# Optimization experiments

Measured on AMD Instinct MI355X. Metric: run time of the kernel, lower is better.

Reference implementation:

```python
import jax, jax.numpy as jnp
import numpy as np

S, B, L, D, H, NOP = 4, 8, 512, 128, 128, 64  # segments, batch, seg_len, input_dim, hidden, n_operators
W = S * L  # 2048 total words
FT = 0.1   # forget-gate floor


def _norm_mat(m):
    # divide each row by its count of nonzero entries (torch normalize_matrix)
    cnt = (m != 0).sum(-1, keepdims=True).astype(m.dtype)
    return m / (cnt + 1e-30)


def _l2(x):
    return x / (jnp.linalg.norm(x, axis=-1, keepdims=True) + 1e-30)


def setup_inputs() -> dict:
    key = jax.random.key(0)
    ks = jax.random.split(key, 16)
    word_outputs = jax.random.normal(ks[0], (S, B, L, D), jnp.float32)
    node_hidden = jax.random.normal(ks[1], (B, D), jnp.float32)
    op_embedding = jax.random.normal(ks[2], (B, NOP, D), jnp.float32)
    word_operator = (jax.random.uniform(ks[3], (B, W, NOP)) < 0.05).astype(jnp.float32)
    word_word = (jax.random.uniform(ks[4], (B, W, W)) < 0.02).astype(jnp.float32)
    depend_relation = (jax.random.uniform(ks[5], (S, B, L, L)) < 0.05).astype(jnp.float32)
    word_exist_matrix = (jax.random.uniform(ks[6], (B, W, W)) < 0.9).astype(jnp.float32)
    word_exist_sequence = (jax.random.uniform(ks[7], (B, W)) < 0.9).astype(jnp.float32)
    goal_word = (jax.random.uniform(ks[8], (B, W)) < 0.2).astype(jnp.float32)

    def lin(k, fi, fo):
        k1, k2 = jax.random.split(k)
        s = 1.0 / np.sqrt(fi).astype(np.float32)
        return (jax.random.uniform(k1, (fi, fo), jnp.float32, -s, s),
                jax.random.uniform(k2, (fo,), jnp.float32, -s, s))

    o_w_W, o_w_b = lin(ks[9], D, H)
    wk_W, wk_b = lin(ks[10], D, H)
    ws_W, ws_b = lin(ks[11], D, H)
    up_W, up_b = lin(ks[12], 3 * H, D)
    wg_W, wg_b = lin(ks[13], D, D)
    fg_W, fg_b = lin(ks[14], 2 * D, D)
    return dict(word_outputs=word_outputs, node_hidden=node_hidden, op_embedding=op_embedding,
                word_operator=word_operator, word_word=word_word, depend_relation=depend_relation,
                word_exist_matrix=word_exist_matrix, word_exist_sequence=word_exist_sequence,
                goal_word=goal_word, o_w_W=o_w_W, o_w_b=o_w_b, wk_W=wk_W, wk_b=wk_b,
                ws_W=ws_W, ws_b=ws_b, up_W=up_W, up_b=up_b, wg_W=wg_W, wg_b=wg_b,
                fg_W=fg_W, fg_b=fg_b)


def reference(word_outputs, node_hidden, op_embedding, word_operator, word_word,
              depend_relation, word_exist_matrix, word_exist_sequence, goal_word,
              o_w_W, o_w_b, wk_W, wk_b, ws_W, ws_b, up_W, up_b, wg_W, wg_b, fg_W, fg_b):
    # cat(word_outputs, dim=1) -> [B, W, D]
    all_word = word_outputs.transpose(1, 0, 2, 3).reshape(B, W, D)
    # operator aggregation: [B,W,NOP] @ o_w(op_embedding) -> [B,W,H], L2-normalized
    word_o = _l2(jnp.einsum('bwo,boh->bwh', word_operator, op_embedding @ o_w_W + o_w_b))
    # knowledge aggregation over masked word-word adjacency
    adj_k = _norm_mat(word_word * word_exist_matrix)
    word_w_k = _l2(jnp.einsum('bvw,bwh->bvh', adj_k, all_word @ wk_W + wk_b))
    # per-segment dependency aggregation, then concat along word dim
    seg = jnp.einsum('sbij,sbjh->sbih', _norm_mat(depend_relation), word_outputs @ ws_W + ws_b)
    word_w_s = _l2(seg.transpose(1, 0, 2, 3).reshape(B, W, H))
    neighbor = jnp.concatenate([word_o, word_w_k, word_w_s], axis=-1)  # [B, W, 3H]
    word_updated = jax.nn.relu(neighbor @ up_W + up_b)  # [B, W, D]
    # goal pooling: bmm([B,1,W],[B,W,D]) -> [B,D]
    gw = _norm_mat(goal_word * word_exist_sequence)
    goal_w = jnp.einsum('bw,bwd->bd', gw, word_updated)
    goal_updated = jax.nn.relu(goal_w @ wg_W + wg_b)
    forget = jax.nn.sigmoid(jnp.concatenate([goal_w, node_hidden], axis=-1) @ fg_W + fg_b)
    return jnp.maximum(forget, FT) * node_hidden + (1.0 - forget) * goal_updated
```

## Files before the change

kernel.cpp:

```cpp
#include <hip/hip_runtime.h>
#include <math.h>

#define Sn 4
#define Bn 8
#define Ln 512
#define Dn 128
#define Hn 128
#define NOPn 64
#define Wn 2048


__device__ __forceinline__ float bf2f(unsigned short u) {
    return __uint_as_float(((unsigned int)u) << 16);
}
__device__ __forceinline__ unsigned short f2bf(float f) {
    unsigned int u = __float_as_uint(f);
    return (unsigned short)((u + 0x7FFFu + ((u >> 16) & 1u)) >> 16);
}

__global__ __launch_bounds__(256) void prep_k(const float* __restrict__ A,
                                              const float* __restrict__ W1,
                                              const float* __restrict__ W2,
                                              const float* __restrict__ b1,
                                              const float* __restrict__ b2,
                                              unsigned short* __restrict__ C1,
                                              unsigned short* __restrict__ C2,
                                              const float* __restrict__ ope,
                                              const float* __restrict__ owW,
                                              const float* __restrict__ owb,
                                              unsigned short* __restrict__ oph,
                                              const float* __restrict__ goal,
                                              const float* __restrict__ wes,
                                              int* __restrict__ widx,
                                              int* __restrict__ wcnt) {
    __shared__ __align__(16) float lA[32][68];
    __shared__ __align__(16) float lW1[32][132];
    __shared__ __align__(16) float lW2[32][132];
    __shared__ int cnt;
    const int bid = blockIdx.x, tid = threadIdx.x;

    if (bid < 256) {
        const int m0 = bid * 64;
        float acc1[4][8] = {}, acc2[4][8] = {};
        const int r0 = (tid & 15) * 4;
        const int h0 = (tid >> 4) * 8;
        for (int k0 = 0; k0 < 128; k0 += 32) {
            __syncthreads();
            {
                const int r = tid >> 2, kk = (tid & 3) * 8;
                const float* src = A + (size_t)(m0 + r) * 128 + (k0 + kk);
                float4 v0 = reinterpret_cast<const float4*>(src)[0];
                float4 v1 = reinterpret_cast<const float4*>(src)[1];
                lA[kk + 0][r] = v0.x; lA[kk + 1][r] = v0.y;
                lA[kk + 2][r] = v0.z; lA[kk + 3][r] = v0.w;
                lA[kk + 4][r] = v1.x; lA[kk + 5][r] = v1.y;
                lA[kk + 6][r] = v1.z; lA[kk + 7][r] = v1.w;
            }
            {
                const int kk = tid >> 3, hh = (tid & 7) * 16;
                const float* s1 = W1 + (size_t)(k0 + kk) * 128 + hh;
                const float* s2 = W2 + (size_t)(k0 + kk) * 128 + hh;
#pragma unroll
                for (int q = 0; q < 4; ++q) {
                    float4 v1 = reinterpret_cast<const float4*>(s1)[q];
                    float4 v2 = reinterpret_cast<const float4*>(s2)[q];
                    lW1[kk][hh + 4 * q + 0] = v1.x; lW1[kk][hh + 4 * q + 1] = v1.y;
                    lW1[kk][hh + 4 * q + 2] = v1.z; lW1[kk][hh + 4 * q + 3] = v1.w;
                    lW2[kk][hh + 4 * q + 0] = v2.x; lW2[kk][hh + 4 * q + 1] = v2.y;
                    lW2[kk][hh + 4 * q + 2] = v2.z; lW2[kk][hh + 4 * q + 3] = v2.w;
                }
            }
            __syncthreads();
#pragma unroll
            for (int k = 0; k < 32; ++k) {
                float4 a   = *reinterpret_cast<const float4*>(&lA[k][r0]);
                float4 w10 = *reinterpret_cast<const float4*>(&lW1[k][h0]);
                float4 w11 = *reinterpret_cast<const float4*>(&lW1[k][h0 + 4]);
                float4 w20 = *reinterpret_cast<const float4*>(&lW2[k][h0]);
                float4 w21 = *reinterpret_cast<const float4*>(&lW2[k][h0 + 4]);
                float av[4] = {a.x, a.y, a.z, a.w};
                float wv1[8] = {w10.x, w10.y, w10.z, w10.w, w11.x, w11.y, w11.z, w11.w};
                float wv2[8] = {w20.x, w20.y, w20.z, w20.w, w21.x, w21.y, w21.z, w21.w};
#pragma unroll
                for (int i = 0; i < 4; ++i)
#pragma unroll
                    for (int j = 0; j < 8; ++j) {
                        acc1[i][j] = fmaf(av[i], wv1[j], acc1[i][j]);
                        acc2[i][j] = fmaf(av[i], wv2[j], acc2[i][j]);
                    }
            }
        }
#pragma unroll
        for (int i = 0; i < 4; ++i) {
            alignas(16) unsigned short u1[8], u2[8];
#pragma unroll
            for (int j = 0; j < 8; ++j) {
                u1[j] = f2bf(acc1[i][j] + b1[h0 + j]);
                u2[j] = f2bf(acc2[i][j] + b2[h0 + j]);
            }
            const size_t off = (size_t)(m0 + r0 + i) * 128 + h0;
            *reinterpret_cast<uint4*>(C1 + off) = *reinterpret_cast<const uint4*>(u1);
            *reinterpret_cast<uint4*>(C2 + off) = *reinterpret_cast<const uint4*>(u2);
        }
    } else if (bid < 264) {
        const int m0 = (bid - 256) * 64;
        float acc[4][8] = {};
        const int r0 = (tid & 15) * 4;
        const int h0 = (tid >> 4) * 8;
        for (int k0 = 0; k0 < 128; k0 += 32) {
            __syncthreads();
            {
                const int r = tid >> 2, kk = (tid & 3) * 8;
                const float* src = ope + (size_t)(m0 + r) * 128 + (k0 + kk);
                float4 v0 = reinterpret_cast<const float4*>(src)[0];
                float4 v1 = reinterpret_cast<const float4*>(src)[1];
                lA[kk + 0][r] = v0.x; lA[kk + 1][r] = v0.y;
                lA[kk + 2][r] = v0.z; lA[kk + 3][r] = v0.w;
                lA[kk + 4][r] = v1.x; lA[kk + 5][r] = v1.y;
                lA[kk + 6][r] = v1.z; lA[kk + 7][r] = v1.w;
            }
            {
                const int kk = tid >> 3, hh = (tid & 7) * 16;
                const float* src = owW + (size_t)(k0 + kk) * 128 + hh;
#pragma unroll
                for (int q = 0; q < 4; ++q) {
                    float4 v = reinterpret_cast<const float4*>(src)[q];
                    lW1[kk][hh + 4 * q + 0] = v.x; lW1[kk][hh + 4 * q + 1] = v.y;
                    lW1[kk][hh + 4 * q + 2] = v.z; lW1[kk][hh + 4 * q + 3] = v.w;
                }
            }
            __syncthreads();
#pragma unroll
            for (int k = 0; k < 32; ++k) {
                float4 a  = *reinterpret_cast<const float4*>(&lA[k][r0]);
                float4 w0 = *reinterpret_cast<const float4*>(&lW1[k][h0]);
                float4 w1 = *reinterpret_cast<const float4*>(&lW1[k][h0 + 4]);
                float av[4] = {a.x, a.y, a.z, a.w};
                float wv[8] = {w0.x, w0.y, w0.z, w0.w, w1.x, w1.y, w1.z, w1.w};
#pragma unroll
                for (int i = 0; i < 4; ++i)
#pragma unroll
                    for (int j = 0; j < 8; ++j) acc[i][j] = fmaf(av[i], wv[j], acc[i][j]);
            }
        }
#pragma unroll
        for (int i = 0; i < 4; ++i) {
            alignas(16) unsigned short us[8];
#pragma unroll
            for (int j = 0; j < 8; ++j) us[j] = f2bf(acc[i][j] + owb[h0 + j]);
            *reinterpret_cast<uint4*>(oph + (size_t)(m0 + r0 + i) * 128 + h0) =
                *reinterpret_cast<const uint4*>(us);
        }
    } else {
        const int b = bid - 264;
        if (tid == 0) cnt = 0;
        __syncthreads();
#pragma unroll
        for (int j = 0; j < 8; ++j) {
            const int w = tid * 8 + j;
            if (goal[b * Wn + w] != 0.f && wes[b * Wn + w] != 0.f) {
                const int p = atomicAdd(&cnt, 1);
                if (p < 1024) widx[b * 1024 + p] = w;
            }
        }
        __syncthreads();
        if (tid == 0) wcnt[b] = cnt < 1024 ? cnt : 1024;
    }
}

__global__ __launch_bounds__(256) void mega_agg(const int* __restrict__ widx,
                                                const int* __restrict__ wcnt,
                                                const float* __restrict__ ww,
                                                const float* __restrict__ wem,
                                                const float* __restrict__ dep,
                                                const float* __restrict__ wop,
                                                const unsigned short* __restrict__ oph,
                                                const unsigned short* __restrict__ wkh,
                                                const unsigned short* __restrict__ wsh,
                                                unsigned short* __restrict__ nbc) {
    const int slot = blockIdx.x;
    const int b = slot >> 10, i = slot & 1023;
    if (i >= wcnt[b]) return;
    const int w_dst = widx[slot];
    const int t = threadIdx.x;
    const int lane = t & 63, wv = t >> 6;

    __shared__ int kidx[512];
    __shared__ int keep[512];
    __shared__ int sidx[256];
    __shared__ int kn, sn;
    __shared__ float part1[4][128];
    __shared__ float part2[4][128];
    if (t == 0) { kn = 0; sn = 0; }
    __syncthreads();

    const float* wwr = ww + ((size_t)(b * Wn + w_dst)) * Wn;
#pragma unroll
    for (int q = 0; q < 2; ++q) {
        const int e0 = q * 1024 + t * 4;
        float4 v = *reinterpret_cast<const float4*>(wwr + e0);
        float vv[4] = {v.x, v.y, v.z, v.w};
#pragma unroll
        for (int j = 0; j < 4; ++j)
            if (vv[j] != 0.f) {
                int p = atomicAdd(&kn, 1);
                if (p < 512) kidx[p] = e0 + j;
            }
    }
    const int sD = w_dst >> 9, lD = w_dst & 511;
    if (t < 128) {
        const float* dr = dep + ((size_t)((sD * Bn + b) * Ln + lD)) * Ln + t * 4;
        float4 v = *reinterpret_cast<const float4*>(dr);
        float vv[4] = {v.x, v.y, v.z, v.w};
#pragma unroll
        for (int j = 0; j < 4; ++j)
            if (vv[j] != 0.f) {
                int p = atomicAdd(&sn, 1);
                if (p < 256) sidx[p] = t * 4 + j;
            }
    }
    float m_op = 0.f;
    if (wv == 3) m_op = wop[((size_t)(b * Wn + w_dst)) * NOPn + lane];
    __syncthreads();

    const int nk = kn < 512 ? kn : 512;
    const int ns = sn < 256 ? sn : 256;
    for (int p = t; p < nk; p += 256)
        keep[p] = (wem[((size_t)(b * Wn + w_dst)) * Wn + kidx[p]] != 0.f) ? 1 : 0;
    __syncthreads();

    {
        float a0 = 0.f, a1 = 0.f;
        for (int p = wv; p < nk; p += 4)
            if (keep[p]) {
                const int w = kidx[p];
                const int s = w >> 9, l = w & 511;
                ushort2 x = *reinterpret_cast<const ushort2*>(
                    wkh + ((size_t)((s * Bn + b) * Ln + l)) * Hn + 2 * lane);
                a0 += bf2f(x.x);
                a1 += bf2f(x.y);
            }
        part1[wv][2 * lane]     = a0;
        part1[wv][2 * lane + 1] = a1;
    }
    {
        const unsigned short* base = wsh + (size_t)((sD * Bn + b) * Ln) * Hn + 2 * lane;
        float a0 = 0.f, a1 = 0.f;
        for (int p = wv; p < ns; p += 4) {
            ushort2 x = *reinterpret_cast<const ushort2*>(base + (size_t)sidx[p] * Hn);
            a0 += bf2f(x.x);
            a1 += bf2f(x.y);
        }
        part2[wv][2 * lane]     = a0;
        part2[wv][2 * lane + 1] = a1;
    }
    if (wv == 3) {
        unsigned long long bal = __ballot(m_op != 0.f);
        float a0 = 0.f, a1 = 0.f;
        const unsigned short* base = oph + (size_t)b * NOPn * Hn + 2 * lane;
        while (bal) {
            const int o = __ffsll(bal) - 1;
            bal &= bal - 1;
            ushort2 v = *reinterpret_cast<const ushort2*>(base + o * Hn);
            a0 += bf2f(v.x);
            a1 += bf2f(v.y);
        }
        float ss = a0 * a0 + a1 * a1;
#pragma unroll
        for (int off = 1; off < 64; off <<= 1) ss += __shfl_xor(ss, off);
        const float sc = 1.f / (sqrtf(ss) + 1e-30f);
        ushort2 o2 = {f2bf(a0 * sc), f2bf(a1 * sc)};
        *reinterpret_cast<ushort2*>(nbc + (size_t)slot * 384 + 2 * lane) = o2;
    }
    __syncthreads();

    if (wv == 0) {
        float s0 = 0.f, s1 = 0.f;
#pragma unroll
        for (int q = 0; q < 4; ++q) {
            s0 += part1[q][2 * lane];
            s1 += part1[q][2 * lane + 1];
        }
        float ss = s0 * s0 + s1 * s1;
#pragma unroll
        for (int off = 1; off < 64; off <<= 1) ss += __shfl_xor(ss, off);
        const float sc = 1.f / (sqrtf(ss) + 1e-30f);
        ushort2 o2 = {f2bf(s0 * sc), f2bf(s1 * sc)};
        *reinterpret_cast<ushort2*>(nbc + (size_t)slot * 384 + 128 + 2 * lane) = o2;
    } else if (wv == 1) {
        float s0 = 0.f, s1 = 0.f;
#pragma unroll
        for (int q = 0; q < 4; ++q) {
            s0 += part2[q][2 * lane];
            s1 += part2[q][2 * lane + 1];
        }
        float ss = s0 * s0 + s1 * s1;
#pragma unroll
        for (int off = 1; off < 64; off <<= 1) ss += __shfl_xor(ss, off);
        const float sc = 1.f / (sqrtf(ss) + 1e-30f);
        ushort2 o2 = {f2bf(s0 * sc), f2bf(s1 * sc)};
        *reinterpret_cast<ushort2*>(nbc + (size_t)slot * 384 + 256 + 2 * lane) = o2;
    }
}

__global__ __launch_bounds__(256) void up_gemm_c(const unsigned short* __restrict__ A,
                                                 const float* __restrict__ Wm,
                                                 const float* __restrict__ bias,
                                                 const int* __restrict__ wcnt,
                                                 float* __restrict__ C) {
    const int m0 = blockIdx.x * 64;
    if ((m0 & 1023) >= wcnt[m0 >> 10]) return;
    __shared__ __align__(16) float lA[32][68];
    __shared__ __align__(16) float lW[32][132];
    const int tid = threadIdx.x;
    float acc[4][8] = {};
    const int r0 = (tid & 15) * 4;
    const int h0 = (tid >> 4) * 8;
    for (int k0 = 0; k0 < 384; k0 += 32) {
        __syncthreads();
        {
            const int r = tid >> 2, kk = (tid & 3) * 8;
            const unsigned short* src = A + (size_t)(m0 + r) * 384 + (k0 + kk);
            alignas(16) unsigned short us[8];
            *reinterpret_cast<uint4*>(us) = *reinterpret_cast<const uint4*>(src);
#pragma unroll
            for (int j = 0; j < 8; ++j) lA[kk + j][r] = bf2f(us[j]);
        }
        {
            const int kk = tid >> 3, hh = (tid & 7) * 16;
            const float* src = Wm + (size_t)(k0 + kk) * 128 + hh;
#pragma unroll
            for (int q = 0; q < 4; ++q) {
                float4 v = reinterpret_cast<const float4*>(src)[q];
                lW[kk][hh + 4 * q + 0] = v.x; lW[kk][hh + 4 * q + 1] = v.y;
                lW[kk][hh + 4 * q + 2] = v.z; lW[kk][hh + 4 * q + 3] = v.w;
            }
        }
        __syncthreads();
#pragma unroll
        for (int k = 0; k < 32; ++k) {
            float4 a  = *reinterpret_cast<const float4*>(&lA[k][r0]);
            float4 w0 = *reinterpret_cast<const float4*>(&lW[k][h0]);
            float4 w1 = *reinterpret_cast<const float4*>(&lW[k][h0 + 4]);
            float av[4] = {a.x, a.y, a.z, a.w};
            float wv[8] = {w0.x, w0.y, w0.z, w0.w, w1.x, w1.y, w1.z, w1.w};
#pragma unroll
            for (int i = 0; i < 4; ++i)
#pragma unroll
                for (int j = 0; j < 8; ++j) acc[i][j] = fmaf(av[i], wv[j], acc[i][j]);
        }
    }
#pragma unroll
    for (int i = 0; i < 4; ++i) {
        float o[8];
#pragma unroll
        for (int j = 0; j < 8; ++j) o[j] = fmaxf(acc[i][j] + bias[h0 + j], 0.f);
        float* dst = C + (size_t)(m0 + r0 + i) * 128 + h0;
        *reinterpret_cast<float4*>(dst)     = reinterpret_cast<float4&>(o[0]);
        *reinterpret_cast<float4*>(dst + 4) = reinterpret_cast<float4&>(o[4]);
    }
}

__global__ __launch_bounds__(1024) void final3_k(const int* __restrict__ wcnt,
                                                 const float* __restrict__ wuc,
                                                 const float* __restrict__ nh,
                                                 const float* __restrict__ wgW,
                                                 const float* __restrict__ wgb,
                                                 const float* __restrict__ fgW,
                                                 const float* __restrict__ fgb,
                                                 float* __restrict__ out) {
    const int b = blockIdx.x, t = threadIdx.x;
    const int d = t & 127, sl = t >> 7;
    __shared__ float red[1024];
    __shared__ float gw[Dn], nhs[Dn];
    const int n = wcnt[b];
    float acc = 0.f;
    for (int p = sl; p < n; p += 8) acc += wuc[((size_t)(b * 1024 + p)) * Dn + d];
    red[t] = acc;
    __syncthreads();
    for (int s = 512; s >= 128; s >>= 1) {
        if (t < s) red[t] += red[t + s];
        __syncthreads();
    }
    if (t < 128) {
        gw[t] = red[t] / ((float)n + 1e-30f);
        nhs[t] = nh[b * Dn + t];
    }
    __syncthreads();
    float pg = 0.f;
    for (int k = sl * 16; k < sl * 16 + 16; ++k) pg = fmaf(gw[k], wgW[k * Dn + d], pg);
    red[t] = pg;
    __syncthreads();
    for (int s = 512; s >= 128; s >>= 1) {
        if (t < s) red[t] += red[t + s];
        __syncthreads();
    }
    float gu = 0.f;
    if (t < 128) gu = fmaxf(red[t] + wgb[t], 0.f);
    __syncthreads();
    float pf = 0.f;
    for (int kk = sl * 32; kk < sl * 32 + 32; ++kk) {
        const float x = (kk < 128) ? gw[kk] : nhs[kk - 128];
        pf = fmaf(x, fgW[(size_t)kk * Dn + d], pf);
    }
    red[t] = pf;
    __syncthreads();
    for (int s = 512; s >= 128; s >>= 1) {
        if (t < s) red[t] += red[t + s];
        __syncthreads();
    }
    if (t < 128) {
        const float fg = red[t] + fgb[t];
        const float forget = 1.f / (1.f + expf(-fg));
        out[b * Dn + t] = fmaxf(forget, 0.1f) * nhs[t] + (1.f - forget) * gu;
    }
}

extern "C" void kernel_launch(void* const* d_in, const int* in_sizes, int n_in,
                              void* d_out, int out_size, void* d_ws, size_t ws_size,
                              hipStream_t stream) {
    (void)in_sizes; (void)n_in; (void)out_size; (void)ws_size;
    const float* word_outputs        = (const float*)d_in[0];
    const float* node_hidden         = (const float*)d_in[1];
    const float* op_embedding        = (const float*)d_in[2];
    const float* word_operator       = (const float*)d_in[3];
    const float* word_word           = (const float*)d_in[4];
    const float* depend_relation     = (const float*)d_in[5];
    const float* word_exist_matrix   = (const float*)d_in[6];
    const float* word_exist_sequence = (const float*)d_in[7];
    const float* goal_word           = (const float*)d_in[8];
    const float* o_w_W = (const float*)d_in[9];
    const float* o_w_b = (const float*)d_in[10];
    const float* wk_W  = (const float*)d_in[11];
    const float* wk_b  = (const float*)d_in[12];
    const float* ws_W  = (const float*)d_in[13];
    const float* ws_b  = (const float*)d_in[14];
    const float* up_W  = (const float*)d_in[15];
    const float* up_b  = (const float*)d_in[16];
    const float* wg_W  = (const float*)d_in[17];
    const float* wg_b  = (const float*)d_in[18];
    const float* fg_W  = (const float*)d_in[19];
    const float* fg_b  = (const float*)d_in[20];
    float* out = (float*)d_out;

    char* ws = (char*)d_ws;
    unsigned short* oph = (unsigned short*)(ws + 0);
    unsigned short* wkh = (unsigned short*)(ws + (1u << 20));
    unsigned short* wsh = (unsigned short*)(ws + (5u << 20));
    int* widx           = (int*)(ws + (9u << 20));
    int* wcnt           = (int*)(ws + (9u << 20) + 32768);
    unsigned short* nbc = (unsigned short*)(ws + (10u << 20));
    float* wuc          = (float*)(ws + (17u << 20));

    prep_k<<<272, 256, 0, stream>>>(word_outputs, wk_W, ws_W, wk_b, ws_b, wkh, wsh,
                                    op_embedding, o_w_W, o_w_b, oph,
                                    goal_word, word_exist_sequence, widx, wcnt);
    mega_agg<<<8192, 256, 0, stream>>>(widx, wcnt, word_word, word_exist_matrix,
                                       depend_relation, word_operator, oph, wkh, wsh, nbc);
    up_gemm_c<<<128, 256, 0, stream>>>(nbc, up_W, up_b, wcnt, wuc);
    final3_k<<<8, 1024, 0, stream>>>(wcnt, wuc, node_hidden,
                                     wg_W, wg_b, fg_W, fg_b, out);
}
```

Baseline: 362.5 us.

## Fuse up-projection and goal pooling into aggregation kernel via atomics

Each aggregation block now keeps its 384-wide neighbor vector in shared memory in fp32. It applies the up_W projection and ReLU itself and atomically adds the result into a per-batch goal accumulator. This drops the bf16 neighbor buffer, the separate up-projection GEMM kernel and the large reduction in the final kernel. The cost is that every block reads the full 384x128 up_W from global or L2 instead of sharing it through a tiled GEMM, and the float atomics make the summation order nondeterministic. A simpler 128-thread final kernel finishes the goal and forget gates.

```diff
diff --git a/kernel.cpp b/kernel.cpp
--- a/kernel.cpp
+++ b/kernel.cpp
@@ -32,7 +32,8 @@
                                               const float* __restrict__ goal,
                                               const float* __restrict__ wes,
                                               int* __restrict__ widx,
-                                              int* __restrict__ wcnt) {
+                                              int* __restrict__ wcnt,
+                                              float* __restrict__ gwacc) {
     __shared__ __align__(16) float lA[32][68];
     __shared__ __align__(16) float lW1[32][132];
     __shared__ __align__(16) float lW2[32][132];
@@ -151,7 +152,7 @@
             *reinterpret_cast<uint4*>(oph + (size_t)(m0 + r0 + i) * 128 + h0) =
                 *reinterpret_cast<const uint4*>(us);
         }
-    } else {
+    } else if (bid < 272) {
         const int b = bid - 264;
         if (tid == 0) cnt = 0;
         __syncthreads();
@@ -165,19 +166,23 @@
         }
         __syncthreads();
         if (tid == 0) wcnt[b] = cnt < 1024 ? cnt : 1024;
-    }
-}
-
-__global__ __launch_bounds__(256) void mega_agg(const int* __restrict__ widx,
-                                                const int* __restrict__ wcnt,
-                                                const float* __restrict__ ww,
-                                                const float* __restrict__ wem,
-                                                const float* __restrict__ dep,
-                                                const float* __restrict__ wop,
-                                                const unsigned short* __restrict__ oph,
-                                                const unsigned short* __restrict__ wkh,
-                                                const unsigned short* __restrict__ wsh,
-                                                unsigned short* __restrict__ nbc) {
+    } else {
+        for (int idx = tid; idx < 1024; idx += 256) gwacc[idx] = 0.f;
+    }
+}
+
+__global__ __launch_bounds__(256) void mega_agg2(const int* __restrict__ widx,
+                                                 const int* __restrict__ wcnt,
+                                                 const float* __restrict__ ww,
+                                                 const float* __restrict__ wem,
+                                                 const float* __restrict__ dep,
+                                                 const float* __restrict__ wop,
+                                                 const unsigned short* __restrict__ oph,
+                                                 const unsigned short* __restrict__ wkh,
+                                                 const unsigned short* __restrict__ wsh,
+                                                 const float* __restrict__ upW,
+                                                 const float* __restrict__ upb,
+                                                 float* __restrict__ gwacc) {
     const int slot = blockIdx.x;
     const int b = slot >> 10, i = slot & 1023;
     if (i >= wcnt[b]) return;
@@ -191,6 +196,8 @@
     __shared__ int kn, sn;
     __shared__ float part1[4][128];
     __shared__ float part2[4][128];
+    __shared__ float nbL[384];
+    __shared__ float gpart[256];
     if (t == 0) { kn = 0; sn = 0; }
     __syncthreads();
 
@@ -269,8 +276,8 @@
 #pragma unroll
         for (int off = 1; off < 64; off <<= 1) ss += __shfl_xor(ss, off);
         const float sc = 1.f / (sqrtf(ss) + 1e-30f);
-        ushort2 o2 = {f2bf(a0 * sc), f2bf(a1 * sc)};
-        *reinterpret_cast<ushort2*>(nbc + (size_t)slot * 384 + 2 * lane) = o2;
+        nbL[2 * lane]     = a0 * sc;
+        nbL[2 * lane + 1] = a1 * sc;
     }
     __syncthreads();
 
@@ -285,8 +292,8 @@
 #pragma unroll
         for (int off = 1; off < 64; off <<= 1) ss += __shfl_xor(ss, off);
         const float sc = 1.f / (sqrtf(ss) + 1e-30f);
-        ushort2 o2 = {f2bf(s0 * sc), f2bf(s1 * sc)};
-        *reinterpret_cast<ushort2*>(nbc + (size_t)slot * 384 + 128 + 2 * lane) = o2;
+        nbL[128 + 2 * lane]     = s0 * sc;
+        nbL[128 + 2 * lane + 1] = s1 * sc;
     } else if (wv == 1) {
         float s0 = 0.f, s1 = 0.f;
 #pragma unroll
@@ -298,122 +305,49 @@
 #pragma unroll
         for (int off = 1; off < 64; off <<= 1) ss += __shfl_xor(ss, off);
         const float sc = 1.f / (sqrtf(ss) + 1e-30f);
-        ushort2 o2 = {f2bf(s0 * sc), f2bf(s1 * sc)};
-        *reinterpret_cast<ushort2*>(nbc + (size_t)slot * 384 + 256 + 2 * lane) = o2;
-    }
-}
-
-__global__ __launch_bounds__(256) void up_gemm_c(const unsigned short* __restrict__ A,
-                                                 const float* __restrict__ Wm,
-                                                 const float* __restrict__ bias,
-                                                 const int* __restrict__ wcnt,
-                                                 float* __restrict__ C) {
-    const int m0 = blockIdx.x * 64;
-    if ((m0 & 1023) >= wcnt[m0 >> 10]) return;
-    __shared__ __align__(16) float lA[32][68];
-    __shared__ __align__(16) float lW[32][132];
-    const int tid = threadIdx.x;
-    float acc[4][8] = {};
-    const int r0 = (tid & 15) * 4;
-    const int h0 = (tid >> 4) * 8;
-    for (int k0 = 0; k0 < 384; k0 += 32) {
-        __syncthreads();
-        {
-            const int r = tid >> 2, kk = (tid & 3) * 8;
-            const unsigned short* src = A + (size_t)(m0 + r) * 384 + (k0 + kk);
-            alignas(16) unsigned short us[8];
-            *reinterpret_cast<uint4*>(us) = *reinterpret_cast<const uint4*>(src);
-#pragma unroll
-            for (int j = 0; j < 8; ++j) lA[kk + j][r] = bf2f(us[j]);
-        }
-        {
-            const int kk = tid >> 3, hh = (tid & 7) * 16;
-            const float* src = Wm + (size_t)(k0 + kk) * 128 + hh;
-#pragma unroll
-            for (int q = 0; q < 4; ++q) {
-                float4 v = reinterpret_cast<const float4*>(src)[q];
-                lW[kk][hh + 4 * q + 0] = v.x; lW[kk][hh + 4 * q + 1] = v.y;
-                lW[kk][hh + 4 * q + 2] = v.z; lW[kk][hh + 4 * q + 3] = v.w;
-            }
-        }
-        __syncthreads();
-#pragma unroll
-        for (int k = 0; k < 32; ++k) {
-            float4 a  = *reinterpret_cast<const float4*>(&lA[k][r0]);
-            float4 w0 = *reinterpret_cast<const float4*>(&lW[k][h0]);
-            float4 w1 = *reinterpret_cast<const float4*>(&lW[k][h0 + 4]);
-            float av[4] = {a.x, a.y, a.z, a.w};
-            float wv[8] = {w0.x, w0.y, w0.z, w0.w, w1.x, w1.y, w1.z, w1.w};
-#pragma unroll
-            for (int i = 0; i < 4; ++i)
-#pragma unroll
-                for (int j = 0; j < 8; ++j) acc[i][j] = fmaf(av[i], wv[j], acc[i][j]);
-        }
-    }
-#pragma unroll
-    for (int i = 0; i < 4; ++i) {
-        float o[8];
-#pragma unroll
-        for (int j = 0; j < 8; ++j) o[j] = fmaxf(acc[i][j] + bias[h0 + j], 0.f);
-        float* dst = C + (size_t)(m0 + r0 + i) * 128 + h0;
-        *reinterpret_cast<float4*>(dst)     = reinterpret_cast<float4&>(o[0]);
-        *reinterpret_cast<float4*>(dst + 4) = reinterpret_cast<float4&>(o[4]);
-    }
-}
-
-__global__ __launch_bounds__(1024) void final3_k(const int* __restrict__ wcnt,
-                                                 const float* __restrict__ wuc,
-                                                 const float* __restrict__ nh,
-                                                 const float* __restrict__ wgW,
-                                                 const float* __restrict__ wgb,
-                                                 const float* __restrict__ fgW,
-                                                 const float* __restrict__ fgb,
-                                                 float* __restrict__ out) {
+        nbL[256 + 2 * lane]     = s0 * sc;
+        nbL[256 + 2 * lane + 1] = s1 * sc;
+    }
+    __syncthreads();
+
+    {
+        const int d = t & 127, half = t >> 7;
+        float acc = 0.f;
+        const float* wp = upW + (size_t)(half * 192) * 128 + d;
+#pragma unroll 8
+        for (int k = 0; k < 192; ++k)
+            acc = fmaf(nbL[half * 192 + k], wp[(size_t)k * 128], acc);
+        gpart[t] = acc;
+    }
+    __syncthreads();
+    if (t < 128) {
+        const float g = fmaxf(gpart[t] + gpart[t + 128] + upb[t], 0.f);
+        atomicAdd(&gwacc[b * 128 + t], g);
+    }
+}
+
+__global__ __launch_bounds__(128) void final4_k(const int* __restrict__ wcnt,
+                                                const float* __restrict__ gwacc,
+                                                const float* __restrict__ nh,
+                                                const float* __restrict__ wgW,
+                                                const float* __restrict__ wgb,
+                                                const float* __restrict__ fgW,
+                                                const float* __restrict__ fgb,
+                                                float* __restrict__ out) {
     const int b = blockIdx.x, t = threadIdx.x;
-    const int d = t & 127, sl = t >> 7;
-    __shared__ float red[1024];
     __shared__ float gw[Dn], nhs[Dn];
-    const int n = wcnt[b];
-    float acc = 0.f;
-    for (int p = sl; p < n; p += 8) acc += wuc[((size_t)(b * 1024 + p)) * Dn + d];
-    red[t] = acc;
-    __syncthreads();
-    for (int s = 512; s >= 128; s >>= 1) {
-        if (t < s) red[t] += red[t + s];
-        __syncthreads();
-    }
-    if (t < 128) {
-        gw[t] = red[t] / ((float)n + 1e-30f);
-        nhs[t] = nh[b * Dn + t];
-    }
-    __syncthreads();
-    float pg = 0.f;
-    for (int k = sl * 16; k < sl * 16 + 16; ++k) pg = fmaf(gw[k], wgW[k * Dn + d], pg);
-    red[t] = pg;
-    __syncthreads();
-    for (int s = 512; s >= 128; s >>= 1) {
-        if (t < s) red[t] += red[t + s];
-        __syncthreads();
-    }
-    float gu = 0.f;
-    if (t < 128) gu = fmaxf(red[t] + wgb[t], 0.f);
-    __syncthreads();
-    float pf = 0.f;
-    for (int kk = sl * 32; kk < sl * 32 + 32; ++kk) {
-        const float x = (kk < 128) ? gw[kk] : nhs[kk - 128];
-        pf = fmaf(x, fgW[(size_t)kk * Dn + d], pf);
-    }
-    red[t] = pf;
-    __syncthreads();
-    for (int s = 512; s >= 128; s >>= 1) {
-        if (t < s) red[t] += red[t + s];
-        __syncthreads();
-    }
-    if (t < 128) {
-        const float fg = red[t] + fgb[t];
-        const float forget = 1.f / (1.f + expf(-fg));
-        out[b * Dn + t] = fmaxf(forget, 0.1f) * nhs[t] + (1.f - forget) * gu;
-    }
+    const float inv = 1.f / ((float)wcnt[b] + 1e-30f);
+    gw[t]  = gwacc[b * Dn + t] * inv;
+    nhs[t] = nh[b * Dn + t];
+    __syncthreads();
+    float gu = wgb[t];
+    for (int d = 0; d < Dn; ++d) gu = fmaf(gw[d], wgW[d * Dn + t], gu);
+    gu = fmaxf(gu, 0.f);
+    float fg = fgb[t];
+    for (int d = 0; d < Dn; ++d) fg = fmaf(gw[d], fgW[d * Dn + t], fg);
+    for (int d = 0; d < Dn; ++d) fg = fmaf(nhs[d], fgW[(Dn + d) * Dn + t], fg);
+    const float forget = 1.f / (1.f + expf(-fg));
+    out[b * Dn + t] = fmaxf(forget, 0.1f) * nhs[t] + (1.f - forget) * gu;
 }
 
 extern "C" void kernel_launch(void* const* d_in, const int* in_sizes, int n_in,
@@ -449,15 +383,14 @@
     unsigned short* wsh = (unsigned short*)(ws + (5u << 20));
     int* widx           = (int*)(ws + (9u << 20));
     int* wcnt           = (int*)(ws + (9u << 20) + 32768);
-    unsigned short* nbc = (unsigned short*)(ws + (10u << 20));
-    float* wuc          = (float*)(ws + (17u << 20));
-
-    prep_k<<<272, 256, 0, stream>>>(word_outputs, wk_W, ws_W, wk_b, ws_b, wkh, wsh,
+    float* gwacc        = (float*)(ws + (9u << 20) + 65536);
+
+    prep_k<<<273, 256, 0, stream>>>(word_outputs, wk_W, ws_W, wk_b, ws_b, wkh, wsh,
                                     op_embedding, o_w_W, o_w_b, oph,
-                                    goal_word, word_exist_sequence, widx, wcnt);
-    mega_agg<<<8192, 256, 0, stream>>>(widx, wcnt, word_word, word_exist_matrix,
-                                       depend_relation, word_operator, oph, wkh, wsh, nbc);
-    up_gemm_c<<<128, 256, 0, stream>>>(nbc, up_W, up_b, wcnt, wuc);
-    final3_k<<<8, 1024, 0, stream>>>(wcnt, wuc, node_hidden,
-                                     wg_W, wg_b, fg_W, fg_b, out);
-}
+                                    goal_word, word_exist_sequence, widx, wcnt, gwacc);
+    mega_agg2<<<8192, 256, 0, stream>>>(widx, wcnt, word_word, word_exist_matrix,
+                                        depend_relation, word_operator, oph, wkh, wsh,
+                                        up_W, up_b, gwacc);
+    final4_k<<<8, 128, 0, stream>>>(wcnt, gwacc, node_hidden,
+                                    wg_W, wg_b, fg_W, fg_b, out);
+}
```

Measured after the change: 355.5 us, median of 2. No clear change (-1.9%).
